# Kernel tuning notes

Hardware: AMD Instinct MI355X
Metric: run time of the kernel (lower is better)

The kernel has to match this reference:

```python
import jax, jax.numpy as jnp
import numpy as np

DIM = 1024
HEADS = 16
DIM_HEAD = 64
INNER = HEADS * DIM_HEAD  # 1024
MLP = 4096
EPS = 1e-5


def setup_inputs() -> dict:
    key = jax.random.key(0)
    ks = jax.random.split(key, 8)
    s = lambda fan_in: 1.0 / np.sqrt(fan_in)
    return {
        "x": jax.random.normal(ks[0], (4, 2048, DIM), dtype=jnp.float32),
        "ln1_g": jnp.ones((DIM,), jnp.float32),
        "ln1_b": jnp.zeros((DIM,), jnp.float32),
        "w_qkv": jax.random.normal(ks[1], (DIM, 3 * INNER), jnp.float32) * s(DIM),
        "w_out": jax.random.normal(ks[2], (INNER, DIM), jnp.float32) * s(INNER),
        "b_out": jnp.zeros((DIM,), jnp.float32),
        "ln2_g": jnp.ones((DIM,), jnp.float32),
        "ln2_b": jnp.zeros((DIM,), jnp.float32),
        "w1": jax.random.normal(ks[3], (DIM, MLP), jnp.float32) * s(DIM),
        "b1": jnp.zeros((MLP,), jnp.float32),
        "w2": jax.random.normal(ks[4], (MLP, DIM), jnp.float32) * s(MLP),
        "b2": jnp.zeros((DIM,), jnp.float32),
    }


def _layernorm(x, g, b):
    mu = jnp.mean(x, axis=-1, keepdims=True)
    var = jnp.mean(jnp.square(x - mu), axis=-1, keepdims=True)
    return (x - mu) * jax.lax.rsqrt(var + EPS) * g + b


def _block(x, ln1_g, ln1_b, w_qkv, w_out, b_out, ln2_g, ln2_b, w1, b1, w2, b2):
    # pre-norm attention
    h = _layernorm(x, ln1_g, ln1_b)
    qkv = h @ w_qkv  # [b, n, 3*inner]
    q, k, v = jnp.split(qkv, 3, axis=-1)
    def heads(t):  # b n (h d) -> b h n d
        b, n, _ = t.shape
        return t.reshape(b, n, HEADS, DIM_HEAD).transpose(0, 2, 1, 3)
    q, k, v = heads(q), heads(k), heads(v)
    scale = DIM_HEAD ** -0.5
    dots = jnp.einsum("bhnd,bhmd->bhnm", q, k) * scale
    attn = jax.nn.softmax(dots, axis=-1)
    out = jnp.einsum("bhnm,bhmd->bhnd", attn, v)
    b, _, n, _ = out.shape
    out = out.transpose(0, 2, 1, 3).reshape(b, n, INNER)
    x = out @ w_out + b_out + x
    # pre-norm FFN
    h = _layernorm(x, ln2_g, ln2_b)
    h = jax.nn.gelu(h @ w1 + b1, approximate=False)
    return h @ w2 + b2 + x


def reference(x, ln1_g, ln1_b, w_qkv, w_out, b_out, ln2_g, ln2_b, w1, b1, w2, b2):
    return _block(x, ln1_g, ln1_b, w_qkv, w_out, b_out, ln2_g, ln2_b, w1, b1, w2, b2)
```

## Files before the change

kernel.cpp:

```cpp
#include <hip/hip_runtime.h>
#include <hip/hip_bf16.h>
#include <math.h>


typedef __bf16 bf16;
typedef __bf16 bf16x8 __attribute__((ext_vector_type(8)));
typedef __bf16 bf16x4 __attribute__((ext_vector_type(4)));
typedef float  f32x4  __attribute__((ext_vector_type(4)));
typedef unsigned int u32;

#define MFMA_16x16x32(a, b, c) __builtin_amdgcn_mfma_f32_16x16x32_bf16((a), (b), (c), 0, 0, 0)

__device__ __forceinline__ void gl_lds16(const void* g, void* l) {
    __builtin_amdgcn_global_load_lds(
        (const __attribute__((address_space(1))) u32*)g,
        (__attribute__((address_space(3))) u32*)l, 16, 0, 0);
}

__device__ __forceinline__ float fast_gelu(float x) {
    const float u = x * (0.7978845608028654f + 0.03567740814183f * x * x);
    const float e = __builtin_amdgcn_exp2f(u * 2.8853900817779268f);
    return x * e * __builtin_amdgcn_rcpf(e + 1.0f);
}

__global__ __launch_bounds__(256) void transpose_f32_bf16(
    const float* __restrict__ in, bf16* __restrict__ out, int R, int C)
{
    __shared__ float tile[32][33];
    const int cb = blockIdx.x * 32, rb = blockIdx.y * 32;
    const int c = threadIdx.x & 31, r0 = threadIdx.x >> 5;
#pragma unroll
    for (int i = 0; i < 4; ++i) {
        int r = r0 + i * 8;
        tile[r][c] = in[(size_t)(rb + r) * C + cb + c];
    }
    __syncthreads();
#pragma unroll
    for (int i = 0; i < 4; ++i) {
        int rr = r0 + i * 8;
        out[(size_t)(cb + rr) * R + rb + c] = (bf16)tile[c][rr];
    }
}

__global__ __launch_bounds__(256) void transpose_v(
    const bf16* __restrict__ qkv, bf16* __restrict__ VT)
{
    __shared__ float tile[32][33];
    const int tokb = blockIdx.x * 32;
    const int db   = blockIdx.y * 32;
    const int bh   = blockIdx.z;
    const int b = bh >> 4, h = bh & 15;
    const int c = threadIdx.x & 31, r0 = threadIdx.x >> 5;
#pragma unroll
    for (int i = 0; i < 4; ++i) {
        int r = r0 + i * 8;
        tile[r][c] = (float)qkv[(size_t)(b * 2048 + tokb + r) * 3072 + 2048 + h * 64 + db + c];
    }
    __syncthreads();
#pragma unroll
    for (int i = 0; i < 4; ++i) {
        int rr = r0 + i * 8;
        VT[((size_t)bh * 64 + db + rr) * 2048 + tokb + c] = (bf16)tile[c][rr];
    }
}

__global__ __launch_bounds__(256) void ln_kernel(
    const float* __restrict__ x, const float* __restrict__ g,
    const float* __restrict__ b, bf16* __restrict__ out)
{
    const int lane = threadIdx.x & 63;
    const int wv   = threadIdx.x >> 6;
    const size_t token = (size_t)blockIdx.x * 4 + wv;
    const float* xr = x + token * 1024;
    float4 v[4];
    float s = 0.f, ss = 0.f;
#pragma unroll
    for (int c = 0; c < 4; ++c) {
        v[c] = *(const float4*)(xr + c * 256 + lane * 4);
        s  += v[c].x + v[c].y + v[c].z + v[c].w;
        ss += v[c].x * v[c].x + v[c].y * v[c].y + v[c].z * v[c].z + v[c].w * v[c].w;
    }
#pragma unroll
    for (int off = 32; off > 0; off >>= 1) {
        s  += __shfl_xor(s, off);
        ss += __shfl_xor(ss, off);
    }
    const float mu  = s * (1.0f / 1024.0f);
    const float var = ss * (1.0f / 1024.0f) - mu * mu;
    const float rs  = rsqrtf(var + 1e-5f);
    bf16* orow = out + token * 1024;
#pragma unroll
    for (int c = 0; c < 4; ++c) {
        float4 gg = *(const float4*)(g + c * 256 + lane * 4);
        float4 bb = *(const float4*)(b + c * 256 + lane * 4);
        bf16x4 o;
        o[0] = (bf16)((v[c].x - mu) * rs * gg.x + bb.x);
        o[1] = (bf16)((v[c].y - mu) * rs * gg.y + bb.y);
        o[2] = (bf16)((v[c].z - mu) * rs * gg.z + bb.z);
        o[3] = (bf16)((v[c].w - mu) * rs * gg.w + bb.w);
        *(bf16x4*)(orow + c * 256 + lane * 4) = o;
    }
}

template <int EPI>
__global__ __launch_bounds__(256, 4) void gemm_bt(
    const bf16* __restrict__ A, const bf16* __restrict__ Bt,
    const float* __restrict__ bias, const float* __restrict__ resid,
    void* __restrict__ outp, int M, int N, int K)
{
    __shared__ __align__(16) bf16 sA[128 * 64];
    __shared__ __align__(16) bf16 sB[128 * 64];

    const int tid  = threadIdx.x;
    const int lane = tid & 63;
    const int wv   = tid >> 6;
    const int quad = lane >> 4;
    const int l16  = lane & 15;

    const int id  = blockIdx.x;
    const int xcd = id & 7, j = id >> 3;
    const int M0 = (xcd * 8 + (j & 7)) * 128;
    const int N0 = (j >> 3) * 128;

    const int wm = (wv >> 1) * 64;
    const int wn = (wv & 1) * 64;

    f32x4 acc[4][4] = {};

    const bf16* paG[4];
    const bf16* pbG[4];
#pragma unroll
    for (int c = 0; c < 4; ++c) {
        const int f = c * 256 + tid;
        const int row = f >> 3;
        const int gch = (f & 7) ^ (row & 7);
        paG[c] = A  + (size_t)(M0 + row) * K + gch * 8;
        pbG[c] = Bt + (size_t)(N0 + row) * K + gch * 8;
    }

    const int sw = l16 & 7;

    for (int k0 = 0; k0 < K; k0 += 64) {
        __syncthreads();
#pragma unroll
        for (int c = 0; c < 4; ++c) {
            const int f8 = (c * 256 + tid) * 8;
            gl_lds16(paG[c] + k0, sA + f8);
            gl_lds16(pbG[c] + k0, sB + f8);
        }
        __syncthreads();

#pragma unroll
        for (int s = 0; s < 2; ++s) {
            const int chp = (s * 4 + quad) ^ sw;
            bf16x8 af[4], bfr[4];
#pragma unroll
            for (int t = 0; t < 4; ++t)
                af[t] = *(const bf16x8*)(sA + ((wm + t * 16 + l16) << 6) + chp * 8);
#pragma unroll
            for (int t = 0; t < 4; ++t)
                bfr[t] = *(const bf16x8*)(sB + ((wn + t * 16 + l16) << 6) + chp * 8);
#pragma unroll
            for (int tm = 0; tm < 4; ++tm)
#pragma unroll
                for (int tn = 0; tn < 4; ++tn)
                    acc[tm][tn] = MFMA_16x16x32(bfr[tn], af[tm], acc[tm][tn]);
        }
    }

#pragma unroll
    for (int tm = 0; tm < 4; ++tm) {
        const int row = M0 + wm + tm * 16 + l16;
#pragma unroll
        for (int tn = 0; tn < 4; ++tn) {
            const int col = N0 + wn + tn * 16 + quad * 4;
            const size_t idx = (size_t)row * N + col;
            const f32x4 v = acc[tm][tn];
            if (EPI == 0) {
                bf16x4 o;
#pragma unroll
                for (int r = 0; r < 4; ++r) o[r] = (bf16)v[r];
                *(bf16x4*)((bf16*)outp + idx) = o;
            } else if (EPI == 1) {
                const f32x4 b4 = *(const f32x4*)(bias + col);
                const f32x4 r4 = *(const f32x4*)(resid + idx);
                *(f32x4*)((float*)outp + idx) = v + b4 + r4;
            } else {
                const f32x4 b4 = *(const f32x4*)(bias + col);
                bf16x4 o;
#pragma unroll
                for (int r = 0; r < 4; ++r) o[r] = (bf16)fast_gelu(v[r] + b4[r]);
                *(bf16x4*)((bf16*)outp + idx) = o;
            }
        }
    }
}

__global__ __launch_bounds__(256, 4) void attn_kernel(
    const bf16* __restrict__ qkv, const bf16* __restrict__ VT,
    bf16* __restrict__ attn_out)
{
    __shared__ __align__(16) bf16 sK[4096];
    __shared__ __align__(16) bf16 sV[4096];
    __shared__ __align__(16) bf16 sP[4][32][72];

    const int bh = blockIdx.y, b = bh >> 4, h = bh & 15;
    const int tid = threadIdx.x, lane = tid & 63, wv = tid >> 6;
    const int quad = lane >> 4, l16 = lane & 15;
    const size_t tok0 = (size_t)b * 2048;
    const int q0 = blockIdx.x * 128 + wv * 32;

    bf16x8 qf[2][2];
#pragma unroll
    for (int mi = 0; mi < 2; ++mi)
#pragma unroll
        for (int c = 0; c < 2; ++c) {
            bf16x8 t = *(const bf16x8*)(qkv + (tok0 + q0 + mi * 16 + l16) * 3072 + h * 64 + c * 32 + quad * 8);
#pragma unroll
            for (int j = 0; j < 8; ++j) t[j] = (bf16)((float)t[j] * 0.18033688011112042f);
            qf[mi][c] = t;
        }

    f32x4 o[2][4] = {};
    float l[2][4] = {};

    const int fA = tid, fB = tid + 256;
    const int cKA = fA >> 8, keyA = (fA >> 2) & 63, qcA = fA & 3;
    const int cKB = fB >> 8, keyB = (fB >> 2) & 63, qcB = fB & 3;
    const int dVA = fA >> 3, ccA = fA & 7;
    const int dVB = fB >> 3, ccB = fB & 7;
    const bf16* Kb = qkv + 1024 + h * 64;
    const bf16* Vb = VT + (size_t)bh * 64 * 2048;

    for (int kt = 0; kt < 32; ++kt) {
        const int kb = kt * 64;
        __syncthreads();
        gl_lds16(Kb + (tok0 + kb + keyA) * 3072 + cKA * 32 + ((qcA ^ (keyA & 3)) * 8), sK + fA * 8);
        gl_lds16(Kb + (tok0 + kb + keyB) * 3072 + cKB * 32 + ((qcB ^ (keyB & 3)) * 8), sK + fB * 8);
        gl_lds16(Vb + (size_t)dVA * 2048 + kb + ((ccA ^ (dVA & 7)) * 8), sV + fA * 8);
        gl_lds16(Vb + (size_t)dVB * 2048 + kb + ((ccB ^ (dVB & 7)) * 8), sV + fB * 8);
        __syncthreads();

        f32x4 s[2][4];
#pragma unroll
        for (int ct = 0; ct < 4; ++ct) {
            const int key = ct * 16 + l16;
            const int ch = quad ^ (l16 & 3);
            bf16x8 k0 = *(const bf16x8*)(sK + (key * 4 + ch) * 8);
            bf16x8 k1 = *(const bf16x8*)(sK + (256 + key * 4 + ch) * 8);
#pragma unroll
            for (int mi = 0; mi < 2; ++mi) {
                f32x4 z = {};
                z = MFMA_16x16x32(qf[mi][0], k0, z);
                z = MFMA_16x16x32(qf[mi][1], k1, z);
                s[mi][ct] = z;
            }
        }
#pragma unroll
        for (int mi = 0; mi < 2; ++mi)
#pragma unroll
            for (int ct = 0; ct < 4; ++ct)
#pragma unroll
                for (int r = 0; r < 4; ++r) {
                    const float p = __builtin_amdgcn_exp2f(s[mi][ct][r]);
                    l[mi][r] += p;
                    sP[wv][mi * 16 + quad * 4 + r][ct * 16 + l16] = (bf16)p;
                }
        bf16x8 vb[4][2];
#pragma unroll
        for (int dt = 0; dt < 4; ++dt) {
            const int d = dt * 16 + l16;
            vb[dt][0] = *(const bf16x8*)(sV + (d * 8 + (quad ^ (l16 & 7))) * 8);
            vb[dt][1] = *(const bf16x8*)(sV + (d * 8 + ((quad + 4) ^ (l16 & 7))) * 8);
        }
#pragma unroll
        for (int mi = 0; mi < 2; ++mi) {
            bf16x8 p0 = *(const bf16x8*)&sP[wv][mi * 16 + l16][quad * 8];
            bf16x8 p1 = *(const bf16x8*)&sP[wv][mi * 16 + l16][32 + quad * 8];
#pragma unroll
            for (int dt = 0; dt < 4; ++dt) {
                o[mi][dt] = MFMA_16x16x32(p0, vb[dt][0], o[mi][dt]);
                o[mi][dt] = MFMA_16x16x32(p1, vb[dt][1], o[mi][dt]);
            }
        }
    }

#pragma unroll
    for (int mi = 0; mi < 2; ++mi) {
        float rl[4];
#pragma unroll
        for (int r = 0; r < 4; ++r) {
            float t = l[mi][r];
            t += __shfl_xor(t, 1); t += __shfl_xor(t, 2);
            t += __shfl_xor(t, 4); t += __shfl_xor(t, 8);
            rl[r] = 1.0f / t;
        }
#pragma unroll
        for (int dt = 0; dt < 4; ++dt)
#pragma unroll
            for (int r = 0; r < 4; ++r) {
                const size_t tok = tok0 + q0 + mi * 16 + quad * 4 + r;
                attn_out[tok * 1024 + h * 64 + dt * 16 + l16] = (bf16)(o[mi][dt][r] * rl[r]);
            }
    }
}

extern "C" void kernel_launch(void* const* d_in, const int* in_sizes, int n_in,
                              void* d_out, int out_size, void* d_ws, size_t ws_size,
                              hipStream_t stream)
{
    const float* x     = (const float*)d_in[0];
    const float* ln1_g = (const float*)d_in[1];
    const float* ln1_b = (const float*)d_in[2];
    const float* w_qkv = (const float*)d_in[3];
    const float* w_out = (const float*)d_in[4];
    const float* b_out = (const float*)d_in[5];
    const float* ln2_g = (const float*)d_in[6];
    const float* ln2_b = (const float*)d_in[7];
    const float* w1    = (const float*)d_in[8];
    const float* b1    = (const float*)d_in[9];
    const float* w2    = (const float*)d_in[10];
    const float* b2    = (const float*)d_in[11];
    float* out = (float*)d_out;

    char* ws = (char*)d_ws;
    bf16*  h      = (bf16*)(ws);
    bf16*  big    = (bf16*)(ws + 16777216);
    bf16*  attn_o = (bf16*)(ws + 83886080);
    float* x_mid  = (float*)(ws + 100663296);
    bf16*  VT     = (bf16*)(ws + 100663296);
    bf16*  wT_qkv = (bf16*)(ws + 134217728);
    bf16*  wT_out = (bf16*)(ws + 140509184);
    bf16*  wT_1   = (bf16*)(ws + 142606336);
    bf16*  wT_2   = (bf16*)(ws + 150994944);

    transpose_f32_bf16<<<dim3(3072/32, 1024/32), 256, 0, stream>>>(w_qkv, wT_qkv, 1024, 3072);
    transpose_f32_bf16<<<dim3(1024/32, 1024/32), 256, 0, stream>>>(w_out, wT_out, 1024, 1024);
    transpose_f32_bf16<<<dim3(4096/32, 1024/32), 256, 0, stream>>>(w1,    wT_1,   1024, 4096);
    transpose_f32_bf16<<<dim3(1024/32, 4096/32), 256, 0, stream>>>(w2,    wT_2,   4096, 1024);

    ln_kernel<<<2048, 256, 0, stream>>>(x, ln1_g, ln1_b, h);

    gemm_bt<0><<<64 * 24, 256, 0, stream>>>(h, wT_qkv, nullptr, nullptr, big, 8192, 3072, 1024);

    transpose_v<<<dim3(64, 2, 64), 256, 0, stream>>>(big, VT);

    attn_kernel<<<dim3(16, 64), 256, 0, stream>>>(big, VT, attn_o);

    gemm_bt<1><<<64 * 8, 256, 0, stream>>>(attn_o, wT_out, b_out, x, x_mid, 8192, 1024, 1024);

    ln_kernel<<<2048, 256, 0, stream>>>(x_mid, ln2_g, ln2_b, h);

    gemm_bt<2><<<64 * 32, 256, 0, stream>>>(h, wT_1, b1, nullptr, big, 8192, 4096, 1024);

    gemm_bt<1><<<64 * 8, 256, 0, stream>>>(big, wT_2, b2, x_mid, out, 8192, 1024, 4096);
}
```

Measured before the change: 489.4 us.

## Add 256x256-tile pipelined GEMM for QKV and FFN-up projections

After: 522.7 us. 6.8% more time.

```diff
diff --git a/kernel.cpp b/kernel.cpp
--- a/kernel.cpp
+++ b/kernel.cpp
@@ -185,6 +185,160 @@
                 const f32x4 b4 = *(const f32x4*)(bias + col);
                 const f32x4 r4 = *(const f32x4*)(resid + idx);
                 *(f32x4*)((float*)outp + idx) = v + b4 + r4;
+            } else {
+                const f32x4 b4 = *(const f32x4*)(bias + col);
+                bf16x4 o;
+#pragma unroll
+                for (int r = 0; r < 4; ++r) o[r] = (bf16)fast_gelu(v[r] + b4[r]);
+                *(bf16x4*)((bf16*)outp + idx) = o;
+            }
+        }
+    }
+}
+
+#define BAR256()  asm volatile("s_barrier" ::: "memory")
+#define WAITVM(n) asm volatile("s_waitcnt vmcnt(" #n ")" ::: "memory")
+#define WAITLG()  do { asm volatile("s_waitcnt lgkmcnt(0)" ::: "memory"); \
+                       __builtin_amdgcn_sched_barrier(0); } while (0)
+
+template <int EPI>
+__global__ __launch_bounds__(512, 2) void gemm256(
+    const bf16* __restrict__ A, const bf16* __restrict__ Bt,
+    const float* __restrict__ bias, void* __restrict__ outp,
+    int N, int K)
+{
+    __shared__ __align__(16) bf16 sA[2][16384];
+    __shared__ __align__(16) bf16 sB[2][16384];
+
+    const int tid  = threadIdx.x;
+    const int lane = tid & 63;
+    const int wv   = tid >> 6;
+    const int quad = lane >> 4;
+    const int l16  = lane & 15;
+    const int wr   = wv >> 2;
+    const int wc   = wv & 3;
+
+    const int id = blockIdx.x;
+    const int wg = (id & 7) * ((int)gridDim.x >> 3) + (id >> 3);
+    const int M0 = (wg & 31) * 256;
+    const int N0 = (wg >> 5) * 256;
+
+    const int srow = tid >> 3;
+    const int sch  = (tid & 7) ^ (srow & 7);
+    const bf16* gA = A  + (size_t)(M0 + srow) * K + sch * 8;
+    const bf16* gB = Bt + (size_t)(N0 + srow) * K + sch * 8;
+    const size_t r64  = (size_t)64 * K;
+    const size_t r128 = (size_t)128 * K;
+
+    f32x4 acc[8][4] = {};
+    bf16x8 af[4][2], bf0[2][2], bf1[2][2];
+
+    auto STG = [&](const bf16* g, bf16* l) {
+        gl_lds16(g, l + tid * 8);
+        gl_lds16(g + r64, l + tid * 8 + 4096);
+    };
+    auto LDA = [&](int buf, int mh) {
+#pragma unroll
+        for (int tm = 0; tm < 4; ++tm) {
+            const int row = wr * 128 + mh * 64 + tm * 16 + l16;
+            const bf16* p = &sA[buf][row * 64];
+            const int swz = (row & 7) << 3;
+            af[tm][0] = *(const bf16x8*)(p + (( quad      << 3) ^ swz));
+            af[tm][1] = *(const bf16x8*)(p + (((quad + 4) << 3) ^ swz));
+        }
+    };
+    auto LDB = [&](int buf, int nh, bf16x8 (&bfr)[2][2]) {
+#pragma unroll
+        for (int tn = 0; tn < 2; ++tn) {
+            const int row = wc * 64 + nh * 32 + tn * 16 + l16;
+            const bf16* p = &sB[buf][row * 64];
+            const int swz = (row & 7) << 3;
+            bfr[tn][0] = *(const bf16x8*)(p + (( quad      << 3) ^ swz));
+            bfr[tn][1] = *(const bf16x8*)(p + (((quad + 4) << 3) ^ swz));
+        }
+    };
+    auto MM = [&](int mh, int nh, bf16x8 (&bfr)[2][2]) {
+        __builtin_amdgcn_s_setprio(1);
+#pragma unroll
+        for (int tm = 0; tm < 4; ++tm)
+#pragma unroll
+            for (int tn = 0; tn < 2; ++tn) {
+                f32x4& a = acc[mh * 4 + tm][nh * 2 + tn];
+                a = MFMA_16x16x32(bfr[tn][0], af[tm][0], a);
+                a = MFMA_16x16x32(bfr[tn][1], af[tm][1], a);
+            }
+        __builtin_amdgcn_s_setprio(0);
+    };
+
+    STG(gA,              &sA[0][0]);
+    STG(gA + r128,       &sA[0][8192]);
+    STG(gB,              &sB[0][0]);
+    STG(gB + r128,       &sB[0][8192]);
+    STG(gB + 64,         &sB[1][0]);
+    STG(gB + r128 + 64,  &sB[1][8192]);
+    WAITVM(4);
+    BAR256();
+
+    const int NU = K >> 7;
+#pragma unroll 1
+    for (int u = 0; u < NU; ++u) {
+        const size_t k1 = (size_t)(2 * u + 1) * 64;
+        const size_t k2 = (size_t)(2 * u + 2) * 64;
+        const size_t k3 = (size_t)(2 * u + 3) * 64;
+        const bool more = (u + 1 < NU);
+
+        LDA(0, 0); LDB(0, 0, bf0);
+        STG(gA + k1, &sA[1][0]);
+        BAR256(); WAITLG(); MM(0, 0, bf0); BAR256();
+
+        LDB(0, 1, bf1);
+        STG(gA + r128 + k1, &sA[1][8192]);
+        BAR256(); WAITLG(); MM(0, 1, bf1); BAR256();
+
+        LDA(0, 1);
+        if (more) STG(gB + k2, &sB[0][0]);
+        BAR256(); WAITLG(); MM(1, 1, bf1); BAR256();
+
+        if (more) STG(gB + r128 + k2, &sB[0][8192]);
+        BAR256(); MM(1, 0, bf0);
+        if (more) { WAITVM(4); } else { WAITVM(0); }
+        BAR256();
+
+        LDA(1, 0); LDB(1, 0, bf0);
+        if (more) STG(gA + k2, &sA[0][0]);
+        BAR256(); WAITLG(); MM(0, 0, bf0); BAR256();
+
+        LDB(1, 1, bf1);
+        if (more) STG(gA + r128 + k2, &sA[0][8192]);
+        BAR256(); WAITLG(); MM(0, 1, bf1); BAR256();
+
+        LDA(1, 1);
+        if (more) STG(gB + k3, &sB[1][0]);
+        BAR256(); WAITLG(); MM(1, 1, bf1); BAR256();
+
+        if (more) {
+            STG(gB + r128 + k3, &sB[1][8192]);
+            BAR256(); MM(1, 0, bf0);
+            WAITVM(4);
+            BAR256();
+        } else {
+            BAR256(); MM(1, 0, bf0);
+        }
+    }
+
+#pragma unroll
+    for (int tm = 0; tm < 8; ++tm) {
+        const int row = M0 + wr * 128 + (tm >> 2) * 64 + (tm & 3) * 16 + l16;
+#pragma unroll
+        for (int tn = 0; tn < 4; ++tn) {
+            const int col = N0 + wc * 64 + (tn >> 1) * 32 + (tn & 1) * 16 + quad * 4;
+            const size_t idx = (size_t)row * N + col;
+            const f32x4 v = acc[tm][tn];
+            if (EPI == 0) {
+                bf16x4 o;
+#pragma unroll
+                for (int r = 0; r < 4; ++r) o[r] = (bf16)v[r];
+                *(bf16x4*)((bf16*)outp + idx) = o;
             } else {
                 const f32x4 b4 = *(const f32x4*)(bias + col);
                 bf16x4 o;
@@ -341,7 +495,7 @@
 
     ln_kernel<<<2048, 256, 0, stream>>>(x, ln1_g, ln1_b, h);
 
-    gemm_bt<0><<<64 * 24, 256, 0, stream>>>(h, wT_qkv, nullptr, nullptr, big, 8192, 3072, 1024);
+    gemm256<0><<<384, 512, 0, stream>>>(h, wT_qkv, nullptr, big, 3072, 1024);
 
     transpose_v<<<dim3(64, 2, 64), 256, 0, stream>>>(big, VT);
 
@@ -351,7 +505,7 @@
 
     ln_kernel<<<2048, 256, 0, stream>>>(x_mid, ln2_g, ln2_b, h);
 
-    gemm_bt<2><<<64 * 32, 256, 0, stream>>>(h, wT_1, b1, nullptr, big, 8192, 4096, 1024);
+    gemm256<2><<<512, 512, 0, stream>>>(h, wT_1, b1, big, 4096, 1024);
 
     gemm_bt<1><<<64 * 8, 256, 0, stream>>>(big, wT_2, b2, x_mid, out, 8192, 1024, 4096);
 }
```

## Double query tiles per attention block to reuse K/V tiles and add MFMA priority

Applied to the files above, without the earlier changes.

Result: slower. 517.3 us (+5.7%).

```diff
diff --git a/kernel.cpp b/kernel.cpp
--- a/kernel.cpp
+++ b/kernel.cpp
@@ -196,13 +196,13 @@
     }
 }
 
-__global__ __launch_bounds__(256, 4) void attn_kernel(
+__global__ __launch_bounds__(256, 2) void attn_kernel(
     const bf16* __restrict__ qkv, const bf16* __restrict__ VT,
     bf16* __restrict__ attn_out)
 {
     __shared__ __align__(16) bf16 sK[4096];
     __shared__ __align__(16) bf16 sV[4096];
-    __shared__ __align__(16) bf16 sP[4][32][72];
+    __shared__ __align__(16) bf16 sP[2][4][32][72];
 
     const int bh = blockIdx.y, b = bh >> 4, h = bh & 15;
     const int tid = threadIdx.x, lane = tid & 63, wv = tid >> 6;
@@ -210,19 +210,21 @@
     const size_t tok0 = (size_t)b * 2048;
     const int q0 = blockIdx.x * 128 + wv * 32;
 
-    bf16x8 qf[2][2];
-#pragma unroll
-    for (int mi = 0; mi < 2; ++mi)
-#pragma unroll
-        for (int c = 0; c < 2; ++c) {
-            bf16x8 t = *(const bf16x8*)(qkv + (tok0 + q0 + mi * 16 + l16) * 3072 + h * 64 + c * 32 + quad * 8);
-#pragma unroll
-            for (int j = 0; j < 8; ++j) t[j] = (bf16)((float)t[j] * 0.18033688011112042f);
-            qf[mi][c] = t;
-        }
-
-    f32x4 o[2][4] = {};
-    float l[2][4] = {};
+    bf16x8 qf[2][2][2];
+#pragma unroll
+    for (int qt = 0; qt < 2; ++qt)
+#pragma unroll
+        for (int mi = 0; mi < 2; ++mi)
+#pragma unroll
+            for (int c = 0; c < 2; ++c) {
+                bf16x8 t = *(const bf16x8*)(qkv + (tok0 + q0 + qt * 1024 + mi * 16 + l16) * 3072 + h * 64 + c * 32 + quad * 8);
+#pragma unroll
+                for (int j = 0; j < 8; ++j) t[j] = (bf16)((float)t[j] * 0.18033688011112042f);
+                qf[qt][mi][c] = t;
+            }
+
+    f32x4 o[2][2][4] = {};
+    float l[2][2][4] = {};
 
     const int fA = tid, fB = tid + 256;
     const int cKA = fA >> 8, keyA = (fA >> 2) & 63, qcA = fA & 3;
@@ -241,7 +243,8 @@
         gl_lds16(Vb + (size_t)dVB * 2048 + kb + ((ccB ^ (dVB & 7)) * 8), sV + fB * 8);
         __syncthreads();
 
-        f32x4 s[2][4];
+        f32x4 s[2][2][4];
+        __builtin_amdgcn_s_setprio(1);
 #pragma unroll
         for (int ct = 0; ct < 4; ++ct) {
             const int key = ct * 16 + l16;
@@ -249,23 +252,17 @@
             bf16x8 k0 = *(const bf16x8*)(sK + (key * 4 + ch) * 8);
             bf16x8 k1 = *(const bf16x8*)(sK + (256 + key * 4 + ch) * 8);
 #pragma unroll
-            for (int mi = 0; mi < 2; ++mi) {
-                f32x4 z = {};
-                z = MFMA_16x16x32(qf[mi][0], k0, z);
-                z = MFMA_16x16x32(qf[mi][1], k1, z);
-                s[mi][ct] = z;
-            }
-        }
-#pragma unroll
-        for (int mi = 0; mi < 2; ++mi)
-#pragma unroll
-            for (int ct = 0; ct < 4; ++ct)
-#pragma unroll
-                for (int r = 0; r < 4; ++r) {
-                    const float p = __builtin_amdgcn_exp2f(s[mi][ct][r]);
-                    l[mi][r] += p;
-                    sP[wv][mi * 16 + quad * 4 + r][ct * 16 + l16] = (bf16)p;
+            for (int qt = 0; qt < 2; ++qt)
+#pragma unroll
+                for (int mi = 0; mi < 2; ++mi) {
+                    f32x4 z = {};
+                    z = MFMA_16x16x32(qf[qt][mi][0], k0, z);
+                    z = MFMA_16x16x32(qf[qt][mi][1], k1, z);
+                    s[qt][mi][ct] = z;
                 }
+        }
+        __builtin_amdgcn_s_setprio(0);
+
         bf16x8 vb[4][2];
 #pragma unroll
         for (int dt = 0; dt < 4; ++dt) {
@@ -273,36 +270,54 @@
             vb[dt][0] = *(const bf16x8*)(sV + (d * 8 + (quad ^ (l16 & 7))) * 8);
             vb[dt][1] = *(const bf16x8*)(sV + (d * 8 + ((quad + 4) ^ (l16 & 7))) * 8);
         }
+
+#pragma unroll
+        for (int qt = 0; qt < 2; ++qt) {
+#pragma unroll
+            for (int mi = 0; mi < 2; ++mi)
+#pragma unroll
+                for (int ct = 0; ct < 4; ++ct)
+#pragma unroll
+                    for (int r = 0; r < 4; ++r) {
+                        const float p = __builtin_amdgcn_exp2f(s[qt][mi][ct][r]);
+                        l[qt][mi][r] += p;
+                        sP[qt][wv][mi * 16 + quad * 4 + r][ct * 16 + l16] = (bf16)p;
+                    }
+            __builtin_amdgcn_s_setprio(1);
+#pragma unroll
+            for (int mi = 0; mi < 2; ++mi) {
+                bf16x8 p0 = *(const bf16x8*)&sP[qt][wv][mi * 16 + l16][quad * 8];
+                bf16x8 p1 = *(const bf16x8*)&sP[qt][wv][mi * 16 + l16][32 + quad * 8];
+#pragma unroll
+                for (int dt = 0; dt < 4; ++dt) {
+                    o[qt][mi][dt] = MFMA_16x16x32(p0, vb[dt][0], o[qt][mi][dt]);
+                    o[qt][mi][dt] = MFMA_16x16x32(p1, vb[dt][1], o[qt][mi][dt]);
+                }
+            }
+            __builtin_amdgcn_s_setprio(0);
+        }
+    }
+
+#pragma unroll
+    for (int qt = 0; qt < 2; ++qt)
 #pragma unroll
         for (int mi = 0; mi < 2; ++mi) {
-            bf16x8 p0 = *(const bf16x8*)&sP[wv][mi * 16 + l16][quad * 8];
-            bf16x8 p1 = *(const bf16x8*)&sP[wv][mi * 16 + l16][32 + quad * 8];
-#pragma unroll
-            for (int dt = 0; dt < 4; ++dt) {
-                o[mi][dt] = MFMA_16x16x32(p0, vb[dt][0], o[mi][dt]);
-                o[mi][dt] = MFMA_16x16x32(p1, vb[dt][1], o[mi][dt]);
+            float rl[4];
+#pragma unroll
+            for (int r = 0; r < 4; ++r) {
+                float t = l[qt][mi][r];
+                t += __shfl_xor(t, 1); t += __shfl_xor(t, 2);
+                t += __shfl_xor(t, 4); t += __shfl_xor(t, 8);
+                rl[r] = 1.0f / t;
             }
-        }
-    }
-
-#pragma unroll
-    for (int mi = 0; mi < 2; ++mi) {
-        float rl[4];
-#pragma unroll
-        for (int r = 0; r < 4; ++r) {
-            float t = l[mi][r];
-            t += __shfl_xor(t, 1); t += __shfl_xor(t, 2);
-            t += __shfl_xor(t, 4); t += __shfl_xor(t, 8);
-            rl[r] = 1.0f / t;
-        }
-#pragma unroll
-        for (int dt = 0; dt < 4; ++dt)
-#pragma unroll
-            for (int r = 0; r < 4; ++r) {
-                const size_t tok = tok0 + q0 + mi * 16 + quad * 4 + r;
-                attn_out[tok * 1024 + h * 64 + dt * 16 + l16] = (bf16)(o[mi][dt][r] * rl[r]);
-            }
-    }
+#pragma unroll
+            for (int dt = 0; dt < 4; ++dt)
+#pragma unroll
+                for (int r = 0; r < 4; ++r) {
+                    const size_t tok = tok0 + q0 + qt * 1024 + mi * 16 + quad * 4 + r;
+                    attn_out[tok * 1024 + h * 64 + dt * 16 + l16] = (bf16)(o[qt][mi][dt][r] * rl[r]);
+                }
+        }
 }
 
 extern "C" void kernel_launch(void* const* d_in, const int* in_sizes, int n_in,
@@ -345,7 +360,7 @@
 
     transpose_v<<<dim3(64, 2, 64), 256, 0, stream>>>(big, VT);
 
-    attn_kernel<<<dim3(16, 64), 256, 0, stream>>>(big, VT, attn_o);
+    attn_kernel<<<dim3(8, 64), 256, 0, stream>>>(big, VT, attn_o);
 
     gemm_bt<1><<<64 * 8, 256, 0, stream>>>(attn_o, wT_out, b_out, x, x_mid, 8192, 1024, 1024);
 
```

## Halve queries per wave in attention and raise MFMA priority

Applied to the files above, without the earlier changes.

Result: slower. 542.4 us (+10.8%).

```diff
diff --git a/kernel.cpp b/kernel.cpp
--- a/kernel.cpp
+++ b/kernel.cpp
@@ -202,27 +202,25 @@
 {
     __shared__ __align__(16) bf16 sK[4096];
     __shared__ __align__(16) bf16 sV[4096];
-    __shared__ __align__(16) bf16 sP[4][32][72];
+    __shared__ __align__(16) bf16 sP[4][16][72];
 
     const int bh = blockIdx.y, b = bh >> 4, h = bh & 15;
     const int tid = threadIdx.x, lane = tid & 63, wv = tid >> 6;
     const int quad = lane >> 4, l16 = lane & 15;
     const size_t tok0 = (size_t)b * 2048;
-    const int q0 = blockIdx.x * 128 + wv * 32;
-
-    bf16x8 qf[2][2];
-#pragma unroll
-    for (int mi = 0; mi < 2; ++mi)
-#pragma unroll
-        for (int c = 0; c < 2; ++c) {
-            bf16x8 t = *(const bf16x8*)(qkv + (tok0 + q0 + mi * 16 + l16) * 3072 + h * 64 + c * 32 + quad * 8);
-#pragma unroll
-            for (int j = 0; j < 8; ++j) t[j] = (bf16)((float)t[j] * 0.18033688011112042f);
-            qf[mi][c] = t;
-        }
-
-    f32x4 o[2][4] = {};
-    float l[2][4] = {};
+    const int q0 = blockIdx.x * 64 + wv * 16;
+
+    bf16x8 qf[2];
+#pragma unroll
+    for (int c = 0; c < 2; ++c) {
+        bf16x8 t = *(const bf16x8*)(qkv + (tok0 + q0 + l16) * 3072 + h * 64 + c * 32 + quad * 8);
+#pragma unroll
+        for (int j = 0; j < 8; ++j) t[j] = (bf16)((float)t[j] * 0.18033688011112042f);
+        qf[c] = t;
+    }
+
+    f32x4 o[4] = {};
+    float l[4] = {};
 
     const int fA = tid, fB = tid + 256;
     const int cKA = fA >> 8, keyA = (fA >> 2) & 63, qcA = fA & 3;
@@ -241,31 +239,30 @@
         gl_lds16(Vb + (size_t)dVB * 2048 + kb + ((ccB ^ (dVB & 7)) * 8), sV + fB * 8);
         __syncthreads();
 
-        f32x4 s[2][4];
+        f32x4 s[4];
+        __builtin_amdgcn_s_setprio(1);
 #pragma unroll
         for (int ct = 0; ct < 4; ++ct) {
             const int key = ct * 16 + l16;
             const int ch = quad ^ (l16 & 3);
             bf16x8 k0 = *(const bf16x8*)(sK + (key * 4 + ch) * 8);
             bf16x8 k1 = *(const bf16x8*)(sK + (256 + key * 4 + ch) * 8);
-#pragma unroll
-            for (int mi = 0; mi < 2; ++mi) {
-                f32x4 z = {};
-                z = MFMA_16x16x32(qf[mi][0], k0, z);
-                z = MFMA_16x16x32(qf[mi][1], k1, z);
-                s[mi][ct] = z;
+            f32x4 z = {};
+            z = MFMA_16x16x32(qf[0], k0, z);
+            z = MFMA_16x16x32(qf[1], k1, z);
+            s[ct] = z;
+        }
+        __builtin_amdgcn_s_setprio(0);
+
+#pragma unroll
+        for (int ct = 0; ct < 4; ++ct)
+#pragma unroll
+            for (int r = 0; r < 4; ++r) {
+                const float p = __builtin_amdgcn_exp2f(s[ct][r]);
+                l[r] += p;
+                sP[wv][quad * 4 + r][ct * 16 + l16] = (bf16)p;
             }
-        }
-#pragma unroll
-        for (int mi = 0; mi < 2; ++mi)
-#pragma unroll
-            for (int ct = 0; ct < 4; ++ct)
-#pragma unroll
-                for (int r = 0; r < 4; ++r) {
-                    const float p = __builtin_amdgcn_exp2f(s[mi][ct][r]);
-                    l[mi][r] += p;
-                    sP[wv][mi * 16 + quad * 4 + r][ct * 16 + l16] = (bf16)p;
-                }
+
         bf16x8 vb[4][2];
 #pragma unroll
         for (int dt = 0; dt < 4; ++dt) {
@@ -273,36 +270,32 @@
             vb[dt][0] = *(const bf16x8*)(sV + (d * 8 + (quad ^ (l16 & 7))) * 8);
             vb[dt][1] = *(const bf16x8*)(sV + (d * 8 + ((quad + 4) ^ (l16 & 7))) * 8);
         }
-#pragma unroll
-        for (int mi = 0; mi < 2; ++mi) {
-            bf16x8 p0 = *(const bf16x8*)&sP[wv][mi * 16 + l16][quad * 8];
-            bf16x8 p1 = *(const bf16x8*)&sP[wv][mi * 16 + l16][32 + quad * 8];
-#pragma unroll
-            for (int dt = 0; dt < 4; ++dt) {
-                o[mi][dt] = MFMA_16x16x32(p0, vb[dt][0], o[mi][dt]);
-                o[mi][dt] = MFMA_16x16x32(p1, vb[dt][1], o[mi][dt]);
-            }
-        }
-    }
-
-#pragma unroll
-    for (int mi = 0; mi < 2; ++mi) {
-        float rl[4];
+        bf16x8 p0 = *(const bf16x8*)&sP[wv][l16][quad * 8];
+        bf16x8 p1 = *(const bf16x8*)&sP[wv][l16][32 + quad * 8];
+        __builtin_amdgcn_s_setprio(1);
+#pragma unroll
+        for (int dt = 0; dt < 4; ++dt) {
+            o[dt] = MFMA_16x16x32(p0, vb[dt][0], o[dt]);
+            o[dt] = MFMA_16x16x32(p1, vb[dt][1], o[dt]);
+        }
+        __builtin_amdgcn_s_setprio(0);
+    }
+
+    float rl[4];
+#pragma unroll
+    for (int r = 0; r < 4; ++r) {
+        float t = l[r];
+        t += __shfl_xor(t, 1); t += __shfl_xor(t, 2);
+        t += __shfl_xor(t, 4); t += __shfl_xor(t, 8);
+        rl[r] = 1.0f / t;
+    }
+#pragma unroll
+    for (int dt = 0; dt < 4; ++dt)
 #pragma unroll
         for (int r = 0; r < 4; ++r) {
-            float t = l[mi][r];
-            t += __shfl_xor(t, 1); t += __shfl_xor(t, 2);
-            t += __shfl_xor(t, 4); t += __shfl_xor(t, 8);
-            rl[r] = 1.0f / t;
-        }
-#pragma unroll
-        for (int dt = 0; dt < 4; ++dt)
-#pragma unroll
-            for (int r = 0; r < 4; ++r) {
-                const size_t tok = tok0 + q0 + mi * 16 + quad * 4 + r;
-                attn_out[tok * 1024 + h * 64 + dt * 16 + l16] = (bf16)(o[mi][dt][r] * rl[r]);
-            }
-    }
+            const size_t tok = tok0 + q0 + quad * 4 + r;
+            attn_out[tok * 1024 + h * 64 + dt * 16 + l16] = (bf16)(o[dt][r] * rl[r]);
+        }
 }
 
 extern "C" void kernel_launch(void* const* d_in, const int* in_sizes, int n_in,
@@ -345,7 +338,7 @@
 
     transpose_v<<<dim3(64, 2, 64), 256, 0, stream>>>(big, VT);
 
-    attn_kernel<<<dim3(16, 64), 256, 0, stream>>>(big, VT, attn_o);
+    attn_kernel<<<dim3(32, 64), 256, 0, stream>>>(big, VT, attn_o);
 
     gemm_bt<1><<<64 * 8, 256, 0, stream>>>(attn_o, wT_out, b_out, x, x_mid, 8192, 1024, 1024);
 
```
